# Optimization experiments

Measured on AMD Instinct MI355X. Metric: run time of the kernel, lower is better.

The kernel has to match this reference:

```python
import jax, jax.numpy as jnp
import numpy as np

N, M, D = 8192, 8192, 128
EPS = 1e-9


def setup_inputs() -> dict:
    key = jax.random.key(0)
    k1, k2 = jax.random.split(key)
    X = jax.random.normal(k1, (N, D), dtype=jnp.float32)
    Y = jax.random.normal(k2, (M, D), dtype=jnp.float32)
    sigma = jnp.ones((1,), dtype=jnp.float32)  # bandwidth (self.sigma)
    return {"X": X, "Y": Y, "sigma": sigma}


def reference(X, Y, sigma):
    # l2norm: ||x_i - y_j||^2 = ||x_i||^2 - 2 x_i.y_j + ||y_j||^2
    # (original builds full XX/YY Gram matrices just for their diagonals;
    #  same math via row-wise sums of squares)
    x2 = jnp.sum(X * X, axis=1)          # [n]
    y2 = jnp.sum(Y * Y, axis=1)          # [m]
    xy = jnp.matmul(X, Y.T)              # [n, m]
    dnorm2 = x2[:, None] - 2.0 * xy + y2[None, :]
    sigma2_inv = 1.0 / (sigma[0] ** 2 + EPS)
    K_XY = jnp.exp(-sigma2_inv * dnorm2)  # [n, m]
    return K_XY
```

## Files before the change

### kernel.cpp

```cpp
#include <hip/hip_runtime.h>
#include <stdint.h>

#define D_DIM 128
#define NROW 8192
#define MROW 8192
#define TILE 128
#define OUT_LD 8192
#define NTILE 64

typedef __bf16 bf16x8 __attribute__((ext_vector_type(8)));
typedef float f32x4 __attribute__((ext_vector_type(4)));
typedef unsigned short u16x8 __attribute__((ext_vector_type(8)));

__device__ __forceinline__ unsigned short f32_to_bf16(float f) {
    uint32_t u = __float_as_uint(f);
    u = (u + 0x7FFFu + ((u >> 16) & 1u)) >> 16;
    return (unsigned short)u;
}

__global__ __launch_bounds__(256) void rbf_norms(const float* __restrict__ X,
                                                 const float* __restrict__ Y,
                                                 float* __restrict__ nrm) {
    const int t = threadIdx.x;
    const int w = t >> 6, lane = t & 63;
    const int rid = blockIdx.x * 4 + w;
    const float* src = (rid < NROW) ? (X + (size_t)rid * D_DIM)
                                    : (Y + (size_t)(rid - NROW) * D_DIM);
    float2 v = *(const float2*)(src + 2 * lane);
    float s = v.x * v.x + v.y * v.y;
    #pragma unroll
    for (int off = 32; off > 0; off >>= 1) s += __shfl_xor(s, off, 64);
    if (lane == 0) nrm[rid] = s;
}

__global__ __launch_bounds__(256) void rbf_pack(const float* __restrict__ X,
                                                const float* __restrict__ Y,
                                                unsigned short* __restrict__ Xt,
                                                unsigned short* __restrict__ Yt) {
    const int gid = blockIdx.x * 256 + threadIdx.x;
    const int mat = gid >> 17;
    const int u = gid & 131071;
    const int chunk = u >> 10;
    const int b16 = u & 1023;
    const int tt = chunk >> 1, p = chunk & 1;
    const int r = b16 >> 3;
    const int k2 = (((b16 & 7) << 4) ^ ((r & 7) << 4));
    const int k = k2 >> 1;
    const float* src = (mat ? Y : X) + (size_t)(tt * TILE + r) * D_DIM + p * 64 + k;
    float4 a = *(const float4*)src;
    float4 b = *(const float4*)(src + 4);
    u16x8 h = { f32_to_bf16(a.x), f32_to_bf16(a.y), f32_to_bf16(a.z), f32_to_bf16(a.w),
                f32_to_bf16(b.x), f32_to_bf16(b.y), f32_to_bf16(b.z), f32_to_bf16(b.w) };
    unsigned short* dst = (mat ? Yt : Xt) + (size_t)chunk * 8192 + (size_t)b16 * 8;
    *(u16x8*)dst = h;
}

__global__ __launch_bounds__(256, 4) void rbf_main(const unsigned short* __restrict__ Xt,
                                                   const unsigned short* __restrict__ Yt,
                                                   const float* __restrict__ sigma,
                                                   const float* __restrict__ nrm,
                                                   float* __restrict__ out) {
    __shared__ unsigned short Xs[8192];
    __shared__ unsigned short Ys[8192];
    __shared__ float x2s[TILE];
    __shared__ float y2s[TILE];

    const int t = threadIdx.x;

    const int flat = blockIdx.y * 64 + blockIdx.x;
    const int nf = (flat & 7) * 512 + (flat >> 3);
    const int tyi = nf >> 6;
    const int txi = nf & 63;
    const int row0 = tyi * TILE;
    const int col0 = txi * TILE;

    if (t < 128) x2s[t] = nrm[row0 + t];
    else         y2s[t - 128] = nrm[NROW + col0 + (t - 128)];

    const int w = t >> 6, ln = t & 63;
    const int quad = ln >> 4, l16 = ln & 15;
    const int wr = (w >> 1) * 64;
    const int wc = (w & 1) * 64;
    const int xorv = (l16 & 7) << 4;

    f32x4 acc[4][4] = {};

    #pragma unroll
    for (int p = 0; p < 2; ++p) {
        const char* gx = (const char*)Xt + ((size_t)(tyi * 2 + p) << 14);
        const char* gy = (const char*)Yt + ((size_t)(txi * 2 + p) << 14);
        #pragma unroll
        for (int i = 0; i < 4; ++i) {
            const int off = ((w * 4 + i) * 64 + ln) * 16;
            const int loff = (w * 4 + i) * 1024;
            __builtin_amdgcn_global_load_lds(
                (const __attribute__((address_space(1))) unsigned int*)(gx + off),
                (__attribute__((address_space(3))) unsigned int*)((char*)Xs + loff),
                16, 0, 0);
            __builtin_amdgcn_global_load_lds(
                (const __attribute__((address_space(1))) unsigned int*)(gy + off),
                (__attribute__((address_space(3))) unsigned int*)((char*)Ys + loff),
                16, 0, 0);
        }
        asm volatile("s_waitcnt vmcnt(0)" ::: "memory");
        __syncthreads();

        #pragma unroll
        for (int ks = 0; ks < 2; ++ks) {
            const int kb = (((ks << 6) | (quad << 4)) ^ xorv);
            bf16x8 ax[4], by[4];
            #pragma unroll
            for (int ti = 0; ti < 4; ++ti)
                ax[ti] = *(const bf16x8*)((const char*)Xs + (wr + ti * 16 + l16) * 128 + kb);
            #pragma unroll
            for (int tj = 0; tj < 4; ++tj)
                by[tj] = *(const bf16x8*)((const char*)Ys + (wc + tj * 16 + l16) * 128 + kb);
            #pragma unroll
            for (int ti = 0; ti < 4; ++ti)
                #pragma unroll
                for (int tj = 0; tj < 4; ++tj)
                    acc[ti][tj] = __builtin_amdgcn_mfma_f32_16x16x32_bf16(by[tj], ax[ti], acc[ti][tj], 0, 0, 0);
        }
        if (p == 0) __syncthreads();
    }

    const float s2 = sigma[0] * sigma[0] + 1e-9f;
    const float cexp = -1.4426950408889634f / s2;

    float x2r[4];
    #pragma unroll
    for (int ti = 0; ti < 4; ++ti) x2r[ti] = x2s[wr + ti * 16 + l16];

    #pragma unroll
    for (int tj = 0; tj < 4; ++tj) {
        f32x4 y2v = *(const f32x4*)(&y2s[wc + tj * 16 + quad * 4]);
        size_t gcol = (size_t)(col0 + wc + tj * 16 + quad * 4);
        #pragma unroll
        for (int ti = 0; ti < 4; ++ti) {
            f32x4 v;
            #pragma unroll
            for (int r = 0; r < 4; ++r) {
                float d = x2r[ti] + y2v[r] - 2.0f * acc[ti][tj][r];
                v[r] = __builtin_amdgcn_exp2f(d * cexp);
            }
            size_t grow = (size_t)(row0 + wr + ti * 16 + l16);
            *(f32x4*)(out + grow * OUT_LD + gcol) = v;
        }
    }
}

extern "C" void kernel_launch(void* const* d_in, const int* in_sizes, int n_in,
                              void* d_out, int out_size, void* d_ws, size_t ws_size,
                              hipStream_t stream) {
    const float* X = (const float*)d_in[0];
    const float* Y = (const float*)d_in[1];
    const float* sigma = (const float*)d_in[2];
    float* nrm = (float*)d_ws;
    unsigned short* Xt = (unsigned short*)((char*)d_ws + 65536);
    unsigned short* Yt = Xt + (size_t)128 * 8192;
    float* out = (float*)d_out;

    rbf_norms<<<(NROW + MROW) / 4, 256, 0, stream>>>(X, Y, nrm);
    rbf_pack<<<1024, 256, 0, stream>>>(X, Y, Xt, Yt);
    rbf_main<<<dim3(MROW / TILE, NROW / TILE), 256, 0, stream>>>(Xt, Yt, sigma, nrm, out);
}
```

Measured before the change: 282.0 us.

## Pack operands in MFMA fragment order, drop LDS staging, fuse norms into pack

The pack kernel now writes bf16 X and Y in the exact per-lane MFMA fragment order, so the main kernel loads its A/B fragments straight from global memory into registers with no LDS staging or barriers. The row-norm computation is folded into the pack kernel, which removes one launch, and the main kernel reads norms directly from global memory. Launch bounds drop to 3 waves per SIMD. This removes LDS traffic and synchronisation, but fragment loads now go through L2/global latency with no explicit prefetch, and occupancy may change.

```diff
diff --git a/kernel.cpp b/kernel.cpp
--- a/kernel.cpp
+++ b/kernel.cpp
@@ -6,7 +6,6 @@
 #define MROW 8192
 #define TILE 128
 #define OUT_LD 8192
-#define NTILE 64
 
 typedef __bf16 bf16x8 __attribute__((ext_vector_type(8)));
 typedef float f32x4 __attribute__((ext_vector_type(4)));
@@ -18,53 +17,47 @@
     return (unsigned short)u;
 }
 
-__global__ __launch_bounds__(256) void rbf_norms(const float* __restrict__ X,
-                                                 const float* __restrict__ Y,
-                                                 float* __restrict__ nrm) {
-    const int t = threadIdx.x;
-    const int w = t >> 6, lane = t & 63;
-    const int rid = blockIdx.x * 4 + w;
-    const float* src = (rid < NROW) ? (X + (size_t)rid * D_DIM)
-                                    : (Y + (size_t)(rid - NROW) * D_DIM);
-    float2 v = *(const float2*)(src + 2 * lane);
-    float s = v.x * v.x + v.y * v.y;
-    #pragma unroll
-    for (int off = 32; off > 0; off >>= 1) s += __shfl_xor(s, off, 64);
-    if (lane == 0) nrm[rid] = s;
-}
-
 __global__ __launch_bounds__(256) void rbf_pack(const float* __restrict__ X,
                                                 const float* __restrict__ Y,
                                                 unsigned short* __restrict__ Xt,
-                                                unsigned short* __restrict__ Yt) {
-    const int gid = blockIdx.x * 256 + threadIdx.x;
+                                                unsigned short* __restrict__ Yt,
+                                                float* __restrict__ nrm) {
+    __shared__ float part[4][16];
+    const int t = threadIdx.x;
+    const int gid = blockIdx.x * 256 + t;
     const int mat = gid >> 17;
     const int u = gid & 131071;
-    const int chunk = u >> 10;
-    const int b16 = u & 1023;
-    const int tt = chunk >> 1, p = chunk & 1;
-    const int r = b16 >> 3;
-    const int k2 = (((b16 & 7) << 4) ^ ((r & 7) << 4));
-    const int k = k2 >> 1;
-    const float* src = (mat ? Y : X) + (size_t)(tt * TILE + r) * D_DIM + p * 64 + k;
+    const int tt = u >> 11;
+    const int ti = (u >> 8) & 7;
+    const int ks = (u >> 6) & 3;
+    const int quad = (u >> 4) & 3;
+    const int l16 = u & 15;
+    const int row = tt * 128 + ti * 16 + l16;
+
+    const float* src = (mat ? Y : X) + (size_t)row * D_DIM + ks * 32 + quad * 8;
     float4 a = *(const float4*)src;
     float4 b = *(const float4*)(src + 4);
     u16x8 h = { f32_to_bf16(a.x), f32_to_bf16(a.y), f32_to_bf16(a.z), f32_to_bf16(a.w),
                 f32_to_bf16(b.x), f32_to_bf16(b.y), f32_to_bf16(b.z), f32_to_bf16(b.w) };
-    unsigned short* dst = (mat ? Yt : Xt) + (size_t)chunk * 8192 + (size_t)b16 * 8;
-    *(u16x8*)dst = h;
+    *(u16x8*)((mat ? Yt : Xt) + (size_t)u * 8) = h;
+
+    float s = a.x*a.x + a.y*a.y + a.z*a.z + a.w*a.w
+            + b.x*b.x + b.y*b.y + b.z*b.z + b.w*b.w;
+    s += __shfl_xor(s, 16, 64);
+    s += __shfl_xor(s, 32, 64);
+    if ((t & 63) < 16) part[t >> 6][t & 15] = s;
+    __syncthreads();
+    if (t < 16) {
+        float tot = part[0][t] + part[1][t] + part[2][t] + part[3][t];
+        nrm[(mat ? NROW : 0) + tt * 128 + ti * 16 + t] = tot;
+    }
 }
 
-__global__ __launch_bounds__(256, 4) void rbf_main(const unsigned short* __restrict__ Xt,
+__global__ __launch_bounds__(256, 3) void rbf_main(const unsigned short* __restrict__ Xt,
                                                    const unsigned short* __restrict__ Yt,
                                                    const float* __restrict__ sigma,
                                                    const float* __restrict__ nrm,
                                                    float* __restrict__ out) {
-    __shared__ unsigned short Xs[8192];
-    __shared__ unsigned short Ys[8192];
-    __shared__ float x2s[TILE];
-    __shared__ float y2s[TILE];
-
     const int t = threadIdx.x;
 
     const int flat = blockIdx.y * 64 + blockIdx.x;
@@ -74,54 +67,30 @@
     const int row0 = tyi * TILE;
     const int col0 = txi * TILE;
 
-    if (t < 128) x2s[t] = nrm[row0 + t];
-    else         y2s[t - 128] = nrm[NROW + col0 + (t - 128)];
-
     const int w = t >> 6, ln = t & 63;
     const int quad = ln >> 4, l16 = ln & 15;
-    const int wr = (w >> 1) * 64;
-    const int wc = (w & 1) * 64;
-    const int xorv = (l16 & 7) << 4;
+    const int wr2 = (w >> 1) * 4;
+    const int wc2 = (w & 1) * 4;
+
+    const char* xb = (const char*)Xt + ((size_t)((tyi * 8 + wr2) * 256 + ln)) * 16;
+    const char* yb = (const char*)Yt + ((size_t)((txi * 8 + wc2) * 256 + ln)) * 16;
 
     f32x4 acc[4][4] = {};
 
     #pragma unroll
-    for (int p = 0; p < 2; ++p) {
-        const char* gx = (const char*)Xt + ((size_t)(tyi * 2 + p) << 14);
-        const char* gy = (const char*)Yt + ((size_t)(txi * 2 + p) << 14);
+    for (int ks = 0; ks < 4; ++ks) {
+        bf16x8 ax[4], by[4];
         #pragma unroll
-        for (int i = 0; i < 4; ++i) {
-            const int off = ((w * 4 + i) * 64 + ln) * 16;
-            const int loff = (w * 4 + i) * 1024;
-            __builtin_amdgcn_global_load_lds(
-                (const __attribute__((address_space(1))) unsigned int*)(gx + off),
-                (__attribute__((address_space(3))) unsigned int*)((char*)Xs + loff),
-                16, 0, 0);
-            __builtin_amdgcn_global_load_lds(
-                (const __attribute__((address_space(1))) unsigned int*)(gy + off),
-                (__attribute__((address_space(3))) unsigned int*)((char*)Ys + loff),
-                16, 0, 0);
-        }
-        asm volatile("s_waitcnt vmcnt(0)" ::: "memory");
-        __syncthreads();
-
+        for (int ti = 0; ti < 4; ++ti)
+            ax[ti] = *(const bf16x8*)(xb + ti * 4096 + ks * 1024);
         #pragma unroll
-        for (int ks = 0; ks < 2; ++ks) {
-            const int kb = (((ks << 6) | (quad << 4)) ^ xorv);
-            bf16x8 ax[4], by[4];
-            #pragma unroll
-            for (int ti = 0; ti < 4; ++ti)
-                ax[ti] = *(const bf16x8*)((const char*)Xs + (wr + ti * 16 + l16) * 128 + kb);
+        for (int tj = 0; tj < 4; ++tj)
+            by[tj] = *(const bf16x8*)(yb + tj * 4096 + ks * 1024);
+        #pragma unroll
+        for (int ti = 0; ti < 4; ++ti)
             #pragma unroll
             for (int tj = 0; tj < 4; ++tj)
-                by[tj] = *(const bf16x8*)((const char*)Ys + (wc + tj * 16 + l16) * 128 + kb);
-            #pragma unroll
-            for (int ti = 0; ti < 4; ++ti)
-                #pragma unroll
-                for (int tj = 0; tj < 4; ++tj)
-                    acc[ti][tj] = __builtin_amdgcn_mfma_f32_16x16x32_bf16(by[tj], ax[ti], acc[ti][tj], 0, 0, 0);
-        }
-        if (p == 0) __syncthreads();
+                acc[ti][tj] = __builtin_amdgcn_mfma_f32_16x16x32_bf16(by[tj], ax[ti], acc[ti][tj], 0, 0, 0);
     }
 
     const float s2 = sigma[0] * sigma[0] + 1e-9f;
@@ -129,12 +98,13 @@
 
     float x2r[4];
     #pragma unroll
-    for (int ti = 0; ti < 4; ++ti) x2r[ti] = x2s[wr + ti * 16 + l16];
+    for (int ti = 0; ti < 4; ++ti)
+        x2r[ti] = nrm[row0 + wr2 * 16 + ti * 16 + l16];
 
     #pragma unroll
     for (int tj = 0; tj < 4; ++tj) {
-        f32x4 y2v = *(const f32x4*)(&y2s[wc + tj * 16 + quad * 4]);
-        size_t gcol = (size_t)(col0 + wc + tj * 16 + quad * 4);
+        f32x4 y2v = *(const f32x4*)(nrm + NROW + col0 + wc2 * 16 + tj * 16 + quad * 4);
+        size_t gcol = (size_t)(col0 + wc2 * 16 + tj * 16 + quad * 4);
         #pragma unroll
         for (int ti = 0; ti < 4; ++ti) {
             f32x4 v;
@@ -143,7 +113,7 @@
                 float d = x2r[ti] + y2v[r] - 2.0f * acc[ti][tj][r];
                 v[r] = __builtin_amdgcn_exp2f(d * cexp);
             }
-            size_t grow = (size_t)(row0 + wr + ti * 16 + l16);
+            size_t grow = (size_t)(row0 + wr2 * 16 + ti * 16 + l16);
             *(f32x4*)(out + grow * OUT_LD + gcol) = v;
         }
     }
@@ -157,10 +127,9 @@
     const float* sigma = (const float*)d_in[2];
     float* nrm = (float*)d_ws;
     unsigned short* Xt = (unsigned short*)((char*)d_ws + 65536);
-    unsigned short* Yt = Xt + (size_t)128 * 8192;
+    unsigned short* Yt = Xt + (size_t)131072 * 8;
     float* out = (float*)d_out;
 
-    rbf_norms<<<(NROW + MROW) / 4, 256, 0, stream>>>(X, Y, nrm);
-    rbf_pack<<<1024, 256, 0, stream>>>(X, Y, Xt, Yt);
+    rbf_pack<<<1024, 256, 0, stream>>>(X, Y, Xt, Yt, nrm);
     rbf_main<<<dim3(MROW / TILE, NROW / TILE), 256, 0, stream>>>(Xt, Yt, sigma, nrm, out);
 }
```

Result: slower. 287.7 us (+2.0%).
